# Optimization experiments

Measured on AMD Instinct MI355X. Metric: run time of the kernel, lower is better.

Reference implementation:

```python
import jax, jax.numpy as jnp
import numpy as np
from jax import lax

B, T, D, H, V, L = 32, 64, 512, 512, 32000, 2
EOS, PAD = 3, 0
SAMPLE_SEED = 42


def setup_inputs() -> dict:
    key = jax.random.key(0)
    ks = jax.random.split(key, 10)
    s = 0.05
    return {
        "input_seq": jax.random.normal(ks[0], (B, T, D), dtype=jnp.float32),
        "h_encode": jax.random.normal(ks[1], (L, B, H), dtype=jnp.float32),
        "c_encode": jax.random.normal(ks[2], (L, B, H), dtype=jnp.float32),
        # stacked per-layer LSTM cell params (layer0 in=D, layer>=1 in=H; D==H so stackable)
        "W_ih": jax.random.normal(ks[3], (L, 4 * H, D), dtype=jnp.float32) * s,
        "W_hh": jax.random.normal(ks[4], (L, 4 * H, H), dtype=jnp.float32) * s,
        "b_ih": jnp.zeros((L, 4 * H), dtype=jnp.float32),
        "b_hh": jnp.zeros((L, 4 * H), dtype=jnp.float32),
        "fc_w": jax.random.normal(ks[5], (V, H), dtype=jnp.float32) * s,
        "fc_b": jnp.zeros((V,), dtype=jnp.float32),
        "embed": jax.random.normal(ks[6], (V, D), dtype=jnp.float32) * s,
    }


def _lstm_cell(x, h, c, wi, wh, bi, bh):
    # gates in torch LSTMCell order: i, f, g, o
    g = x @ wi.T + bi + h @ wh.T + bh  # [B, 4H]
    i, f, gg, o = jnp.split(g, 4, axis=-1)
    i, f, o = jax.nn.sigmoid(i), jax.nn.sigmoid(f), jax.nn.sigmoid(o)
    c2 = f * c + i * jnp.tanh(gg)
    h2 = o * jnp.tanh(c2)
    return h2, c2


def reference(input_seq, h_encode, c_encode, W_ih, W_hh, b_ih, b_hh, fc_w, fc_b, embed):
    n_layers = h_encode.shape[0]
    seq = jnp.swapaxes(input_seq, 0, 1)  # [T, B, D]
    batch = input_seq.shape[0]

    def step(carry, t):
        h, c, finished, x = carry
        inp = x
        hs, cs = [], []
        for l in range(n_layers):  # fixed small layer loop
            hl, cl = _lstm_cell(inp, h[l], c[l], W_ih[l], W_hh[l], b_ih[l], b_hh[l])
            hs.append(hl)
            cs.append(cl)
            inp = hl
        h2 = jnp.stack(hs)
        c2 = jnp.stack(cs)
        logits = inp @ fc_w.T + fc_b  # [B, V]; temperature=1.0 is identity
        key = jax.random.fold_in(jax.random.key(SAMPLE_SEED), t)
        sampled = jax.random.categorical(key, logits, axis=-1)  # multinomial(softmax(logits))
        token = jnp.where(finished, PAD, sampled)
        finished2 = finished | (sampled == EOS)
        next_x = embed[token]  # [B, D] feedback embedding (no teacher forcing)
        return (h2, c2, finished2, next_x), (logits, token)

    carry0 = (h_encode, c_encode, jnp.zeros((batch,), dtype=bool), seq[0])
    _, (logits_t, tokens_t) = lax.scan(step, carry0, jnp.arange(seq.shape[0]))
    outputs = jnp.swapaxes(logits_t, 0, 1)  # [B, T, V]
    tokens = jnp.swapaxes(tokens_t, 0, 1)  # [B, T]
    return outputs, tokens
```

## Files before the change

kernel.cpp:

```cpp
#include <hip/hip_runtime.h>
#include <cstdint>
#include <cstddef>

#define B_  32
#define T_  64
#define D_  512
#define H_  512
#define V_  32000
#define NPART 8

__device__ float g_x[B_ * D_];
__device__ float g_h[2][2 * B_ * H_];
__device__ float g_c[2][2 * B_ * H_];
__device__ float g_pval[B_ * NPART];
__device__ int   g_pidx[B_ * NPART];
__device__ int   g_fin[B_];
__device__ float g_wT[512 * 32000];
__device__ float g_wLT[2][1024 * 2048];
__device__ float g_part[64][B_][2048];
__device__ float g_lpart[8][B_][V_];

__host__ __device__ __forceinline__ void threefry2x32(uint32_t k0, uint32_t k1,
                                                      uint32_t x0, uint32_t x1,
                                                      uint32_t& o0, uint32_t& o1) {
  uint32_t kx = k0 ^ k1 ^ 0x1BD11BDAu;
  x0 += k0; x1 += k1;
#define RND(r) { x0 += x1; x1 = (x1 << (r)) | (x1 >> (32 - (r))); x1 ^= x0; }
  RND(13) RND(15) RND(26) RND(6)  x0 += k1; x1 += kx + 1u;
  RND(17) RND(29) RND(16) RND(24) x0 += kx; x1 += k0 + 2u;
  RND(13) RND(15) RND(26) RND(6)  x0 += k0; x1 += k1 + 3u;
  RND(17) RND(29) RND(16) RND(24) x0 += k1; x1 += kx + 4u;
  RND(13) RND(15) RND(26) RND(6)  x0 += kx; x1 += k0 + 5u;
#undef RND
  o0 = x0; o1 = x1;
}

__device__ __forceinline__ float gumbel_from_u32(uint32_t bits) {
  float f = __uint_as_float((bits >> 9) | 0x3f800000u) - 1.0f;
  const float TINY = 1.1754943508222875e-38f;
  float u = f * (1.0f - TINY) + TINY;
  u = fmaxf(u, TINY);
  return -logf(-logf(u));
}

__device__ __forceinline__ void fma4(float4& a, const float4 w, float s) {
  a.x += w.x * s; a.y += w.y * s; a.z += w.z * s; a.w += w.w * s;
}

__global__ void init_kernel(const float* __restrict__ input_seq,
                            const float* __restrict__ h_enc,
                            const float* __restrict__ c_enc) {
  int i = blockIdx.x * 256 + threadIdx.x;
  if (i < B_ * D_) g_x[i] = input_seq[(size_t)(i >> 9) * (T_ * D_) + (i & 511)];
  if (i < 2 * B_ * H_) { g_h[0][i] = h_enc[i]; g_c[0][i] = c_enc[i]; }
  if (i < B_) g_fin[i] = 0;
}

__global__ void transpose_kernel(const float* __restrict__ src, int R, int which) {
  float* dst;
  switch (which) {
    case 0:  dst = g_wT; break;
    case 1:  dst = g_wLT[0]; break;
    case 2:  dst = g_wLT[0] + 512 * 2048; break;
    case 3:  dst = g_wLT[1]; break;
    default: dst = g_wLT[1] + 512 * 2048; break;
  }
  __shared__ float tile[64][65];
  const int r0 = blockIdx.x * 64;
  const int c0 = blockIdx.y * 64;
  const int tx = threadIdx.x & 63;
  const int ty = threadIdx.x >> 6;
#pragma unroll
  for (int i = 0; i < 16; ++i) {
    const int row = ty + 4 * i;
    tile[row][tx] = src[(size_t)(r0 + row) * 512 + c0 + tx];
  }
  __syncthreads();
#pragma unroll
  for (int i = 0; i < 16; ++i) {
    const int row = ty + 4 * i;
    dst[(size_t)(c0 + row) * R + r0 + tx] = tile[tx][row];
  }
}

__global__ void lstm_part_kernel(int cur, int layer) {
  const int blk = blockIdx.x;
  const int kslo = blk & 7, bg = (blk >> 3) & 3, kshi = blk >> 5;
  const int ks = kslo + 8 * kshi;
  const int tid = threadIdx.x;
  const int b0 = bg * 8;

  const float* z = (ks < 32) ? ((layer == 0) ? g_x : &g_h[cur ^ 1][0])
                             : &g_h[cur][layer * B_ * H_];
  const int k0 = (ks & 31) * 16;

  __shared__ float zs[8][16];
  if (tid < 128) zs[tid >> 4][tid & 15] = z[(b0 + (tid >> 4)) * 512 + k0 + (tid & 15)];
  __syncthreads();

  float4 accA[8], accB[8];
#pragma unroll
  for (int b = 0; b < 8; ++b) { accA[b] = make_float4(0,0,0,0); accB[b] = make_float4(0,0,0,0); }

  for (int kk = 0; kk < 16; ++kk) {
    const float4* w4 = (const float4*)&g_wLT[layer][(size_t)(ks * 16 + kk) * 2048];
    float4 wa = w4[tid], wb = w4[tid + 256];
#pragma unroll
    for (int b = 0; b < 8; ++b) {
      float zb = zs[b][kk];
      fma4(accA[b], wa, zb);
      fma4(accB[b], wb, zb);
    }
  }
#pragma unroll
  for (int b = 0; b < 8; ++b) {
    float4* p = (float4*)&g_part[ks][b0 + b][0];
    p[tid]       = accA[b];
    p[tid + 256] = accB[b];
  }
}

__global__ void lstm_finish_kernel(int cur, int layer,
                                   const float* __restrict__ bih,
                                   const float* __restrict__ bhh) {
  const int gid = blockIdx.x * 256 + threadIdx.x;
  const int b = gid >> 9, j = gid & 511;
  float gi = 0.f, gf = 0.f, gg = 0.f, go = 0.f;
#pragma unroll 8
  for (int ks = 0; ks < 64; ++ks) {
    gi += g_part[ks][b][j];
    gf += g_part[ks][b][512 + j];
    gg += g_part[ks][b][1024 + j];
    go += g_part[ks][b][1536 + j];
  }
  gi += bih[j]          + bhh[j];
  gf += bih[512 + j]    + bhh[512 + j];
  gg += bih[1024 + j]   + bhh[1024 + j];
  go += bih[1536 + j]   + bhh[1536 + j];

  const float* c_in = &g_c[cur][layer * B_ * H_];
  float* h_out = &g_h[cur ^ 1][layer * B_ * H_];
  float* c_out = &g_c[cur ^ 1][layer * B_ * H_];
  float c0 = c_in[b * H_ + j];
  float si = 1.f / (1.f + expf(-gi));
  float sf = 1.f / (1.f + expf(-gf));
  float so = 1.f / (1.f + expf(-go));
  float cn = sf * c0 + si * tanhf(gg);
  float hn = so * tanhf(cn);
  c_out[b * H_ + j] = cn;
  h_out[b * H_ + j] = hn;
}

__global__ void logits_part_kernel(int cur) {
  const int blk = blockIdx.x;
  const int vt = blk % 63, ks = blk / 63;
  const int tid = threadIdx.x;
  const int k0 = ks * 64;

  __shared__ float hs[32 * 64];
  const float* h2 = &g_h[cur ^ 1][B_ * H_];
  {
    float4* d4 = (float4*)hs;
#pragma unroll
    for (int i = 0; i < 2; ++i) {
      const int f4i = tid + i * 256;
      d4[f4i] = ((const float4*)h2)[(f4i >> 4) * 128 + (k0 >> 2) + (f4i & 15)];
    }
  }
  __syncthreads();

  const int v0 = vt * 512 + tid * 2;
  if (v0 >= V_) return;

  float2 acc[32];
#pragma unroll
  for (int b = 0; b < 32; ++b) acc[b] = make_float2(0.f, 0.f);

  for (int k = 0; k < 64; ++k) {
    float2 w = *(const float2*)&g_wT[(size_t)(k0 + k) * V_ + v0];
#pragma unroll
    for (int b = 0; b < 32; ++b) {
      float hb = hs[b * 64 + k];
      acc[b].x += w.x * hb;
      acc[b].y += w.y * hb;
    }
  }
#pragma unroll
  for (int b = 0; b < 32; ++b)
    *(float2*)&g_lpart[ks][b][v0] = acc[b];
}

__global__ void logits_combine_kernel(const float* __restrict__ fc_b,
                                      float* __restrict__ out_logits,
                                      int t, uint32_t key0, uint32_t key1) {
  __shared__ float sv[256];
  __shared__ int   si[256];
  const int b  = blockIdx.x >> 3;
  const int vr = blockIdx.x & 7;
  const int tid = threadIdx.x;
  const int vend = (vr + 1) * 4000;

  float best = -3.0e38f; int bidx = 0x7fffffff;
  for (int it = 0; it < 16; ++it) {
    const int v = vr * 4000 + it * 256 + tid;
    if (v < vend) {
      float s = 0.f;
#pragma unroll
      for (int ks = 0; ks < 8; ++ks) s += g_lpart[ks][b][v];
      float lv = s + fc_b[v];
      out_logits[(size_t)(b * T_ + t) * V_ + v] = lv;
      uint32_t y0, y1;
      threefry2x32(key0, key1, 0u, (uint32_t)(b * V_ + v), y0, y1);
      float val = lv + gumbel_from_u32(y0 ^ y1);
      if (val > best) { best = val; bidx = v; }
    }
  }
  sv[tid] = best; si[tid] = bidx;
  __syncthreads();
  for (int s = 128; s > 0; s >>= 1) {
    if (tid < s) {
      float ov = sv[tid + s]; int oi = si[tid + s];
      if (ov > sv[tid] || (ov == sv[tid] && oi < si[tid])) { sv[tid] = ov; si[tid] = oi; }
    }
    __syncthreads();
  }
  if (tid == 0) { g_pval[b * NPART + vr] = sv[0]; g_pidx[b * NPART + vr] = si[0]; }
}

__global__ void sample_kernel(const float* __restrict__ embed,
                              float* __restrict__ out_tokens, int t) {
  __shared__ int stok;
  const int b = blockIdx.x;
  const int tid = threadIdx.x;
  if (tid == 0) {
    float best = -3.0e38f; int bidx = 0x7fffffff;
    for (int p = 0; p < NPART; ++p) {
      float v = g_pval[b * NPART + p];
      int  ix = g_pidx[b * NPART + p];
      if (v > best || (v == best && ix < bidx)) { best = v; bidx = ix; }
    }
    int sampled = bidx;
    if (sampled < 0) sampled = 0;
    if (sampled >= V_) sampled = V_ - 1;
    int fin = g_fin[b];
    int token = fin ? 0 : sampled;
    out_tokens[b * T_ + t] = (float)token;
    g_fin[b] = fin | (sampled == 3 ? 1 : 0);
    stok = token;
  }
  __syncthreads();
  const int token = stok;
  const float4* er = (const float4*)(embed + (size_t)token * D_);
  float4* xr = (float4*)(g_x + b * D_);
  if (tid < 128) xr[tid] = er[tid];
}

extern "C" void kernel_launch(void* const* d_in, const int* in_sizes, int n_in,
                              void* d_out, int out_size, void* d_ws, size_t ws_size,
                              hipStream_t stream) {
  const float* input_seq = (const float*)d_in[0];
  const float* h_enc = (const float*)d_in[1];
  const float* c_enc = (const float*)d_in[2];
  const float* Wih   = (const float*)d_in[3];
  const float* Whh   = (const float*)d_in[4];
  const float* bih   = (const float*)d_in[5];
  const float* bhh   = (const float*)d_in[6];
  const float* fc_w  = (const float*)d_in[7];
  const float* fc_b  = (const float*)d_in[8];
  const float* embed = (const float*)d_in[9];
  float* out = (float*)d_out;
  float* tok_out = out + (size_t)B_ * T_ * V_;
  (void)d_ws; (void)ws_size;

  init_kernel<<<128, 256, 0, stream>>>(input_seq, h_enc, c_enc);

  transpose_kernel<<<dim3(500, 8), 256, 0, stream>>>(fc_w, 32000, 0);
  transpose_kernel<<<dim3(32, 8),  256, 0, stream>>>(Wih,                      2048, 1);
  transpose_kernel<<<dim3(32, 8),  256, 0, stream>>>(Whh,                      2048, 2);
  transpose_kernel<<<dim3(32, 8),  256, 0, stream>>>(Wih + (size_t)2048 * 512, 2048, 3);
  transpose_kernel<<<dim3(32, 8),  256, 0, stream>>>(Whh + (size_t)2048 * 512, 2048, 4);

  uint32_t keys[T_][2];
  for (int t = 0; t < T_; ++t)
    threefry2x32(0u, 42u, 0u, (uint32_t)t, keys[t][0], keys[t][1]);

  int cur = 0;
  for (int t = 0; t < T_; ++t) {
    lstm_part_kernel<<<256, 256, 0, stream>>>(cur, 0);
    lstm_finish_kernel<<<64, 256, 0, stream>>>(cur, 0, bih, bhh);
    lstm_part_kernel<<<256, 256, 0, stream>>>(cur, 1);
    lstm_finish_kernel<<<64, 256, 0, stream>>>(cur, 1, bih + 2048, bhh + 2048);
    logits_part_kernel<<<504, 256, 0, stream>>>(cur);
    logits_combine_kernel<<<256, 256, 0, stream>>>(fc_b, out, t, keys[t][0], keys[t][1]);
    sample_kernel<<<B_, 256, 0, stream>>>(embed, tok_out, t);
    cur ^= 1;
  }
}
```

Before: 6.051 ms.

## Fuse sampling into LSTM input staging and hoist layer-1 recurrent matmul early

```diff
diff --git a/kernel.cpp b/kernel.cpp
--- a/kernel.cpp
+++ b/kernel.cpp
@@ -7,18 +7,17 @@
 #define D_  512
 #define H_  512
 #define V_  32000
-#define NPART 8
-
-__device__ float g_x[B_ * D_];
+#define GATES 2048
+
 __device__ float g_h[2][2 * B_ * H_];
 __device__ float g_c[2][2 * B_ * H_];
-__device__ float g_pval[B_ * NPART];
-__device__ int   g_pidx[B_ * NPART];
-__device__ int   g_fin[B_];
+__device__ int   g_fin[2][B_];
+__device__ unsigned long long g_best[B_];
 __device__ float g_wT[512 * 32000];
 __device__ float g_wLT[2][1024 * 2048];
-__device__ float g_part[64][B_][2048];
-__device__ float g_lpart[8][B_][V_];
+__device__ float g_part0[16][B_][GATES];
+__device__ float g_part1[24][B_][GATES];
+__device__ float g_lpart[4][B_][V_];
 
 __host__ __device__ __forceinline__ void threefry2x32(uint32_t k0, uint32_t k1,
                                                       uint32_t x0, uint32_t x1,
@@ -43,17 +42,11 @@
   return -logf(-logf(u));
 }
 
-__device__ __forceinline__ void fma4(float4& a, const float4 w, float s) {
-  a.x += w.x * s; a.y += w.y * s; a.z += w.z * s; a.w += w.w * s;
-}
-
-__global__ void init_kernel(const float* __restrict__ input_seq,
-                            const float* __restrict__ h_enc,
+__global__ void init_kernel(const float* __restrict__ h_enc,
                             const float* __restrict__ c_enc) {
   int i = blockIdx.x * 256 + threadIdx.x;
-  if (i < B_ * D_) g_x[i] = input_seq[(size_t)(i >> 9) * (T_ * D_) + (i & 511)];
   if (i < 2 * B_ * H_) { g_h[0][i] = h_enc[i]; g_c[0][i] = c_enc[i]; }
-  if (i < B_) g_fin[i] = 0;
+  if (i < B_) { g_fin[0][i] = 0; g_fin[1][i] = 0; }
 }
 
 __global__ void transpose_kernel(const float* __restrict__ src, int R, int which) {
@@ -83,60 +76,135 @@
   }
 }
 
-__global__ void lstm_part_kernel(int cur, int layer) {
+template<int PER>
+__device__ __forceinline__ void stage_t(float* __restrict__ zs,
+                                        const float* __restrict__ row,
+                                        int kq, int b) {
+#pragma unroll
+  for (int i = 0; i < PER; i += 4) {
+    const float4 v = *(const float4*)&row[kq * PER + i];
+    const int kk = kq * PER + i;
+    zs[(kk + 0) * 32 + b] = v.x;
+    zs[(kk + 1) * 32 + b] = v.y;
+    zs[(kk + 2) * 32 + b] = v.z;
+    zs[(kk + 3) * 32 + b] = v.w;
+  }
+}
+
+template<int KS>
+__device__ __forceinline__ void mm_part(const float* __restrict__ wrow,
+                                        float* __restrict__ pout,
+                                        const float* __restrict__ zs,
+                                        int j0, int tid) {
+  float2 acc[32];
+#pragma unroll
+  for (int b = 0; b < 32; ++b) acc[b] = make_float2(0.f, 0.f);
+#pragma unroll 4
+  for (int k = 0; k < KS; ++k) {
+    const float2 w = *(const float2*)&wrow[(size_t)k * GATES + j0 + 2 * tid];
+    const float4* z4 = (const float4*)&zs[k * 32];
+#pragma unroll
+    for (int bq = 0; bq < 8; ++bq) {
+      const float4 z = z4[bq];
+      acc[bq * 4 + 0].x += w.x * z.x; acc[bq * 4 + 0].y += w.y * z.x;
+      acc[bq * 4 + 1].x += w.x * z.y; acc[bq * 4 + 1].y += w.y * z.y;
+      acc[bq * 4 + 2].x += w.x * z.z; acc[bq * 4 + 2].y += w.y * z.z;
+      acc[bq * 4 + 3].x += w.x * z.w; acc[bq * 4 + 3].y += w.y * z.w;
+    }
+  }
+#pragma unroll
+  for (int b = 0; b < 32; ++b)
+    *(float2*)&pout[(size_t)b * GATES + j0 + 2 * tid] = acc[b];
+}
+
+__device__ __forceinline__ int unpack_v(unsigned long long bb) {
+  int v = (int)(0xFFFFFFFFu - (uint32_t)(bb & 0xFFFFFFFFu));
+  if (v < 0) v = 0;
+  if (v >= V_) v = V_ - 1;
+  return v;
+}
+
+__global__ void parts_a_kernel(int cur, int t,
+                               const float* __restrict__ input_seq,
+                               const float* __restrict__ embed,
+                               float* __restrict__ out_tokens) {
+  __shared__ __align__(16) float zs[64 * 32];
+  __shared__ int stok[B_];
+  const int tid = threadIdx.x;
   const int blk = blockIdx.x;
-  const int kslo = blk & 7, bg = (blk >> 3) & 3, kshi = blk >> 5;
-  const int ks = kslo + 8 * kshi;
-  const int tid = threadIdx.x;
-  const int b0 = bg * 8;
-
-  const float* z = (ks < 32) ? ((layer == 0) ? g_x : &g_h[cur ^ 1][0])
-                             : &g_h[cur][layer * B_ * H_];
-  const int k0 = (ks & 31) * 16;
-
-  __shared__ float zs[8][16];
-  if (tid < 128) zs[tid >> 4][tid & 15] = z[(b0 + (tid >> 4)) * 512 + k0 + (tid & 15)];
+  const int b = tid >> 3, kq = tid & 7;
+
+  if (blk < 64) {
+    const int ks = blk >> 2, jt = blk & 3;
+    const int k0 = ks * 64, j0 = jt * 512;
+    if (k0 < 512) {
+      if (t == 0) {
+        const float* row = &input_seq[(size_t)b * (T_ * D_)];
+        stage_t<8>(zs, row + k0, kq, b);
+      } else {
+        if (tid < B_) {
+          unsigned long long bb = g_best[tid];
+          int v = unpack_v(bb);
+          int fin = g_fin[(t + 1) & 1][tid];
+          int tok = fin ? 0 : v;
+          stok[tid] = tok;
+          if (blk == 0) {
+            out_tokens[(size_t)tid * T_ + (t - 1)] = (float)tok;
+            g_fin[t & 1][tid] = fin | (v == 3 ? 1 : 0);
+          }
+        }
+        __syncthreads();
+        const float* row = &embed[(size_t)stok[b] * D_];
+        stage_t<8>(zs, row + k0, kq, b);
+      }
+    } else {
+      const float* row = &g_h[cur][0 * B_ * H_ + b * H_];
+      stage_t<8>(zs, row + (k0 - 512), kq, b);
+    }
+    __syncthreads();
+    mm_part<64>(&g_wLT[0][(size_t)k0 * GATES], &g_part0[ks][0][0], zs, j0, tid);
+  } else {
+    const int bb2 = blk - 64;
+    const int ks = bb2 >> 2, jt = bb2 & 3;
+    const int k0 = ks * 64, j0 = jt * 512;
+    const float* row = &g_h[cur][1 * B_ * H_ + b * H_];
+    stage_t<8>(zs, row + k0, kq, b);
+    __syncthreads();
+    mm_part<64>(&g_wLT[1][(size_t)(512 + k0) * GATES], &g_part1[16 + ks][0][0],
+                zs, j0, tid);
+  }
+}
+
+__global__ void parts_l1x_kernel(int cur) {
+  __shared__ __align__(16) float zs[32 * 32];
+  const int tid = threadIdx.x;
+  const int ks = blockIdx.x >> 2, jt = blockIdx.x & 3;
+  const int k0 = ks * 32, j0 = jt * 512;
+  const int b = tid >> 3, kq = tid & 7;
+  const float* row = &g_h[cur ^ 1][0 * B_ * H_ + b * H_];
+  stage_t<4>(zs, row + k0, kq, b);
   __syncthreads();
-
-  float4 accA[8], accB[8];
-#pragma unroll
-  for (int b = 0; b < 8; ++b) { accA[b] = make_float4(0,0,0,0); accB[b] = make_float4(0,0,0,0); }
-
-  for (int kk = 0; kk < 16; ++kk) {
-    const float4* w4 = (const float4*)&g_wLT[layer][(size_t)(ks * 16 + kk) * 2048];
-    float4 wa = w4[tid], wb = w4[tid + 256];
-#pragma unroll
-    for (int b = 0; b < 8; ++b) {
-      float zb = zs[b][kk];
-      fma4(accA[b], wa, zb);
-      fma4(accB[b], wb, zb);
-    }
-  }
-#pragma unroll
-  for (int b = 0; b < 8; ++b) {
-    float4* p = (float4*)&g_part[ks][b0 + b][0];
-    p[tid]       = accA[b];
-    p[tid + 256] = accB[b];
-  }
-}
-
-__global__ void lstm_finish_kernel(int cur, int layer,
+  mm_part<32>(&g_wLT[1][(size_t)k0 * GATES], &g_part1[ks][0][0], zs, j0, tid);
+}
+
+__global__ void lstm_finish_kernel(int cur, int layer, int nslots,
                                    const float* __restrict__ bih,
                                    const float* __restrict__ bhh) {
   const int gid = blockIdx.x * 256 + threadIdx.x;
   const int b = gid >> 9, j = gid & 511;
+  const float* P = (layer == 0) ? &g_part0[0][0][0] : &g_part1[0][0][0];
   float gi = 0.f, gf = 0.f, gg = 0.f, go = 0.f;
-#pragma unroll 8
-  for (int ks = 0; ks < 64; ++ks) {
-    gi += g_part[ks][b][j];
-    gf += g_part[ks][b][512 + j];
-    gg += g_part[ks][b][1024 + j];
-    go += g_part[ks][b][1536 + j];
-  }
-  gi += bih[j]          + bhh[j];
-  gf += bih[512 + j]    + bhh[512 + j];
-  gg += bih[1024 + j]   + bhh[1024 + j];
-  go += bih[1536 + j]   + bhh[1536 + j];
+  for (int s = 0; s < nslots; ++s) {
+    const float* p = P + (size_t)s * B_ * GATES + (size_t)b * GATES;
+    gi += p[j];
+    gf += p[512 + j];
+    gg += p[1024 + j];
+    go += p[1536 + j];
+  }
+  gi += bih[j]        + bhh[j];
+  gf += bih[512 + j]  + bhh[512 + j];
+  gg += bih[1024 + j] + bhh[1024 + j];
+  go += bih[1536 + j] + bhh[1536 + j];
 
   const float* c_in = &g_c[cur][layer * B_ * H_];
   float* h_out = &g_h[cur ^ 1][layer * B_ * H_];
@@ -152,20 +220,18 @@
 }
 
 __global__ void logits_part_kernel(int cur) {
+  __shared__ __align__(16) float hs[128 * 32];
   const int blk = blockIdx.x;
   const int vt = blk % 63, ks = blk / 63;
   const int tid = threadIdx.x;
-  const int k0 = ks * 64;
-
-  __shared__ float hs[32 * 64];
-  const float* h2 = &g_h[cur ^ 1][B_ * H_];
+  const int k0 = ks * 128;
+
+  if (blk == 0 && tid < B_) g_best[tid] = 0ull;
+
   {
-    float4* d4 = (float4*)hs;
-#pragma unroll
-    for (int i = 0; i < 2; ++i) {
-      const int f4i = tid + i * 256;
-      d4[f4i] = ((const float4*)h2)[(f4i >> 4) * 128 + (k0 >> 2) + (f4i & 15)];
-    }
+    const int b = tid >> 3, kq = tid & 7;
+    const float* row = &g_h[cur ^ 1][B_ * H_ + b * H_];
+    stage_t<16>(hs, row + k0, kq, b);
   }
   __syncthreads();
 
@@ -175,14 +241,17 @@
   float2 acc[32];
 #pragma unroll
   for (int b = 0; b < 32; ++b) acc[b] = make_float2(0.f, 0.f);
-
-  for (int k = 0; k < 64; ++k) {
-    float2 w = *(const float2*)&g_wT[(size_t)(k0 + k) * V_ + v0];
-#pragma unroll
-    for (int b = 0; b < 32; ++b) {
-      float hb = hs[b * 64 + k];
-      acc[b].x += w.x * hb;
-      acc[b].y += w.y * hb;
+#pragma unroll 4
+  for (int k = 0; k < 128; ++k) {
+    const float2 w = *(const float2*)&g_wT[(size_t)(k0 + k) * V_ + v0];
+    const float4* z4 = (const float4*)&hs[k * 32];
+#pragma unroll
+    for (int bq = 0; bq < 8; ++bq) {
+      const float4 z = z4[bq];
+      acc[bq * 4 + 0].x += w.x * z.x; acc[bq * 4 + 0].y += w.y * z.x;
+      acc[bq * 4 + 1].x += w.x * z.y; acc[bq * 4 + 1].y += w.y * z.y;
+      acc[bq * 4 + 2].x += w.x * z.z; acc[bq * 4 + 2].y += w.y * z.z;
+      acc[bq * 4 + 3].x += w.x * z.w; acc[bq * 4 + 3].y += w.y * z.w;
     }
   }
 #pragma unroll
@@ -193,66 +262,47 @@
 __global__ void logits_combine_kernel(const float* __restrict__ fc_b,
                                       float* __restrict__ out_logits,
                                       int t, uint32_t key0, uint32_t key1) {
-  __shared__ float sv[256];
-  __shared__ int   si[256];
+  __shared__ unsigned long long sv[256];
   const int b  = blockIdx.x >> 3;
   const int vr = blockIdx.x & 7;
   const int tid = threadIdx.x;
   const int vend = (vr + 1) * 4000;
 
-  float best = -3.0e38f; int bidx = 0x7fffffff;
+  unsigned long long best = 0ull;
   for (int it = 0; it < 16; ++it) {
     const int v = vr * 4000 + it * 256 + tid;
     if (v < vend) {
-      float s = 0.f;
-#pragma unroll
-      for (int ks = 0; ks < 8; ++ks) s += g_lpart[ks][b][v];
+      float s = g_lpart[0][b][v] + g_lpart[1][b][v]
+              + g_lpart[2][b][v] + g_lpart[3][b][v];
       float lv = s + fc_b[v];
       out_logits[(size_t)(b * T_ + t) * V_ + v] = lv;
       uint32_t y0, y1;
       threefry2x32(key0, key1, 0u, (uint32_t)(b * V_ + v), y0, y1);
       float val = lv + gumbel_from_u32(y0 ^ y1);
-      if (val > best) { best = val; bidx = v; }
+      uint32_t u = __float_as_uint(val);
+      u ^= (u >> 31) ? 0xFFFFFFFFu : 0x80000000u;
+      unsigned long long pk =
+          ((unsigned long long)u << 32) | (unsigned long long)(0xFFFFFFFFu - (uint32_t)v);
+      if (pk > best) best = pk;
     }
   }
-  sv[tid] = best; si[tid] = bidx;
+  sv[tid] = best;
   __syncthreads();
   for (int s = 128; s > 0; s >>= 1) {
-    if (tid < s) {
-      float ov = sv[tid + s]; int oi = si[tid + s];
-      if (ov > sv[tid] || (ov == sv[tid] && oi < si[tid])) { sv[tid] = ov; si[tid] = oi; }
-    }
+    if (tid < s) { if (sv[tid + s] > sv[tid]) sv[tid] = sv[tid + s]; }
     __syncthreads();
   }
-  if (tid == 0) { g_pval[b * NPART + vr] = sv[0]; g_pidx[b * NPART + vr] = si[0]; }
-}
-
-__global__ void sample_kernel(const float* __restrict__ embed,
-                              float* __restrict__ out_tokens, int t) {
-  __shared__ int stok;
-  const int b = blockIdx.x;
-  const int tid = threadIdx.x;
-  if (tid == 0) {
-    float best = -3.0e38f; int bidx = 0x7fffffff;
-    for (int p = 0; p < NPART; ++p) {
-      float v = g_pval[b * NPART + p];
-      int  ix = g_pidx[b * NPART + p];
-      if (v > best || (v == best && ix < bidx)) { best = v; bidx = ix; }
-    }
-    int sampled = bidx;
-    if (sampled < 0) sampled = 0;
-    if (sampled >= V_) sampled = V_ - 1;
-    int fin = g_fin[b];
-    int token = fin ? 0 : sampled;
-    out_tokens[b * T_ + t] = (float)token;
-    g_fin[b] = fin | (sampled == 3 ? 1 : 0);
-    stok = token;
-  }
-  __syncthreads();
-  const int token = stok;
-  const float4* er = (const float4*)(embed + (size_t)token * D_);
-  float4* xr = (float4*)(g_x + b * D_);
-  if (tid < 128) xr[tid] = er[tid];
+  if (tid == 0) atomicMax(&g_best[b], sv[0]);
+}
+
+__global__ void finalize_kernel(float* __restrict__ out_tokens) {
+  const int tid = threadIdx.x;
+  if (tid < B_) {
+    int v = unpack_v(g_best[tid]);
+    int fin = g_fin[(T_ + 1) & 1][tid];
+    int tok = fin ? 0 : v;
+    out_tokens[(size_t)tid * T_ + (T_ - 1)] = (float)tok;
+  }
 }
 
 extern "C" void kernel_launch(void* const* d_in, const int* in_sizes, int n_in,
@@ -270,9 +320,9 @@
   const float* embed = (const float*)d_in[9];
   float* out = (float*)d_out;
   float* tok_out = out + (size_t)B_ * T_ * V_;
-  (void)d_ws; (void)ws_size;
-
-  init_kernel<<<128, 256, 0, stream>>>(input_seq, h_enc, c_enc);
+  (void)d_ws; (void)ws_size; (void)in_sizes; (void)n_in; (void)out_size;
+
+  init_kernel<<<128, 256, 0, stream>>>(h_enc, c_enc);
 
   transpose_kernel<<<dim3(500, 8), 256, 0, stream>>>(fc_w, 32000, 0);
   transpose_kernel<<<dim3(32, 8),  256, 0, stream>>>(Wih,                      2048, 1);
@@ -286,13 +336,13 @@
 
   int cur = 0;
   for (int t = 0; t < T_; ++t) {
-    lstm_part_kernel<<<256, 256, 0, stream>>>(cur, 0);
-    lstm_finish_kernel<<<64, 256, 0, stream>>>(cur, 0, bih, bhh);
-    lstm_part_kernel<<<256, 256, 0, stream>>>(cur, 1);
-    lstm_finish_kernel<<<64, 256, 0, stream>>>(cur, 1, bih + 2048, bhh + 2048);
-    logits_part_kernel<<<504, 256, 0, stream>>>(cur);
+    parts_a_kernel<<<96, 256, 0, stream>>>(cur, t, input_seq, embed, tok_out);
+    lstm_finish_kernel<<<64, 256, 0, stream>>>(cur, 0, 16, bih, bhh);
+    parts_l1x_kernel<<<64, 256, 0, stream>>>(cur);
+    lstm_finish_kernel<<<64, 256, 0, stream>>>(cur, 1, 24, bih + 2048, bhh + 2048);
+    logits_part_kernel<<<252, 256, 0, stream>>>(cur);
     logits_combine_kernel<<<256, 256, 0, stream>>>(fc_b, out, t, keys[t][0], keys[t][1]);
-    sample_kernel<<<B_, 256, 0, stream>>>(embed, tok_out, t);
     cur ^= 1;
   }
-}
+  finalize_kernel<<<1, 64, 0, stream>>>(tok_out);
+}
```

Result: slower. 6.330 ms (+4.6%).

## Fuse LSTM split-K, logits, and sampling into fewer kernels with atomic argmax

Applied to the files above, without the earlier changes.

```diff
diff --git a/kernel.cpp b/kernel.cpp
--- a/kernel.cpp
+++ b/kernel.cpp
@@ -7,18 +7,14 @@
 #define D_  512
 #define H_  512
 #define V_  32000
-#define NPART 8
-
-__device__ float g_x[B_ * D_];
+#define GATES 2048
+
 __device__ float g_h[2][2 * B_ * H_];
 __device__ float g_c[2][2 * B_ * H_];
-__device__ float g_pval[B_ * NPART];
-__device__ int   g_pidx[B_ * NPART];
-__device__ int   g_fin[B_];
+__device__ int   g_fin[2][B_];
+__device__ unsigned long long g_best2[2][B_][8];
 __device__ float g_wT[512 * 32000];
 __device__ float g_wLT[2][1024 * 2048];
-__device__ float g_part[64][B_][2048];
-__device__ float g_lpart[8][B_][V_];
 
 __host__ __device__ __forceinline__ void threefry2x32(uint32_t k0, uint32_t k1,
                                                       uint32_t x0, uint32_t x1,
@@ -43,17 +39,24 @@
   return -logf(-logf(u));
 }
 
-__device__ __forceinline__ void fma4(float4& a, const float4 w, float s) {
-  a.x += w.x * s; a.y += w.y * s; a.z += w.z * s; a.w += w.w * s;
-}
-
-__global__ void init_kernel(const float* __restrict__ input_seq,
-                            const float* __restrict__ h_enc,
+__device__ __forceinline__ int unpack_v(unsigned long long bb) {
+  int v = (int)(0xFFFFFFFFu - (uint32_t)(bb & 0xFFFFFFFFu));
+  if (v < 0) v = 0;
+  if (v >= V_) v = V_ - 1;
+  return v;
+}
+
+__device__ __forceinline__ unsigned long long ullmax(unsigned long long a,
+                                                     unsigned long long b) {
+  return a > b ? a : b;
+}
+
+__global__ void init_kernel(const float* __restrict__ h_enc,
                             const float* __restrict__ c_enc) {
   int i = blockIdx.x * 256 + threadIdx.x;
-  if (i < B_ * D_) g_x[i] = input_seq[(size_t)(i >> 9) * (T_ * D_) + (i & 511)];
   if (i < 2 * B_ * H_) { g_h[0][i] = h_enc[i]; g_c[0][i] = c_enc[i]; }
-  if (i < B_) g_fin[i] = 0;
+  if (i < B_) { g_fin[0][i] = 0; g_fin[1][i] = 0; }
+  if (i < 2 * B_ * 8) ((unsigned long long*)g_best2)[i] = 0ull;
 }
 
 __global__ void transpose_kernel(const float* __restrict__ src, int R, int which) {
@@ -83,176 +86,188 @@
   }
 }
 
-__global__ void lstm_part_kernel(int cur, int layer) {
-  const int blk = blockIdx.x;
-  const int kslo = blk & 7, bg = (blk >> 3) & 3, kshi = blk >> 5;
-  const int ks = kslo + 8 * kshi;
+__global__ __launch_bounds__(512) void lstm_cell_kernel(
+    int layer, int cur, int tt,
+    const float* __restrict__ input_seq, const float* __restrict__ embed,
+    const float* __restrict__ bih, const float* __restrict__ bhh,
+    float* __restrict__ out_tokens) {
+  __shared__ __align__(16) float zs[16 * 512];
+  __shared__ float gl[4][16][16];
+  __shared__ int stok[16];
   const int tid = threadIdx.x;
-  const int b0 = bg * 8;
-
-  const float* z = (ks < 32) ? ((layer == 0) ? g_x : &g_h[cur ^ 1][0])
-                             : &g_h[cur][layer * B_ * H_];
-  const int k0 = (ks & 31) * 16;
-
-  __shared__ float zs[8][16];
-  if (tid < 128) zs[tid >> 4][tid & 15] = z[(b0 + (tid >> 4)) * 512 + k0 + (tid & 15)];
+  const int jt = blockIdx.x & 31, bh = blockIdx.x >> 5;
+  const int j0 = jt * 16, b0 = bh * 16;
+
+  if (layer == 0 && tt > 0) {
+    const int ps = (tt - 1) & 1;
+    if (tid < 16) {
+      const int b = b0 + tid;
+      unsigned long long m = 0ull;
+#pragma unroll
+      for (int s = 0; s < 8; ++s) m = ullmax(m, g_best2[ps][b][s]);
+      const int v = unpack_v(m);
+      const int fin = g_fin[ps ^ 1][b];
+      const int tok = fin ? 0 : v;
+      stok[tid] = tok;
+      if (jt == 0) {
+        out_tokens[(size_t)b * T_ + (tt - 1)] = (float)tok;
+        g_fin[ps][b] = fin | (v == 3 ? 1 : 0);
+      }
+    }
+    if (jt == 0 && tid < 128)
+      g_best2[tt & 1][b0 + (tid >> 3)][tid & 7] = 0ull;
+    __syncthreads();
+  }
+
+  const int jp = tid & 7, gg_ = (tid >> 3) & 3, lb = tid >> 5;
+  const float* wbase = &g_wLT[layer][(size_t)gg_ * 512 + j0 + jp * 2];
+  float2 acc = make_float2(0.f, 0.f);
+
+  for (int p = 0; p < 2; ++p) {
+    {
+      const int slb = tid & 15, kq = tid >> 4;
+      const float* src;
+      if (layer == 0) {
+        src = (p == 0)
+          ? ((tt == 0) ? &input_seq[(size_t)(b0 + slb) * T_ * D_]
+                       : &embed[(size_t)stok[slb] * D_])
+          : &g_h[cur][0 * B_ * H_ + (b0 + slb) * H_];
+      } else {
+        src = (p == 0) ? &g_h[cur ^ 1][0 * B_ * H_ + (b0 + slb) * H_]
+                       : &g_h[cur][1 * B_ * H_ + (b0 + slb) * H_];
+      }
+#pragma unroll
+      for (int i = 0; i < 16; i += 4) {
+        const float4 v = *(const float4*)&src[kq * 16 + i];
+        *(float4*)&zs[slb * 512 + kq * 16 + i] = v;
+      }
+    }
+    __syncthreads();
+    const float* wrow = wbase + (size_t)p * 512 * GATES;
+    const float* zrow = &zs[lb * 512];
+#pragma unroll 8
+    for (int k = 0; k < 512; ++k) {
+      const float2 w = *(const float2*)&wrow[(size_t)k * GATES];
+      const float z = zrow[k];
+      acc.x += w.x * z; acc.y += w.y * z;
+    }
+    __syncthreads();
+  }
+
+  *(float2*)&gl[gg_][lb][jp * 2] = acc;
   __syncthreads();
-
-  float4 accA[8], accB[8];
-#pragma unroll
-  for (int b = 0; b < 8; ++b) { accA[b] = make_float4(0,0,0,0); accB[b] = make_float4(0,0,0,0); }
-
-  for (int kk = 0; kk < 16; ++kk) {
-    const float4* w4 = (const float4*)&g_wLT[layer][(size_t)(ks * 16 + kk) * 2048];
-    float4 wa = w4[tid], wb = w4[tid + 256];
-#pragma unroll
-    for (int b = 0; b < 8; ++b) {
-      float zb = zs[b][kk];
-      fma4(accA[b], wa, zb);
-      fma4(accB[b], wb, zb);
-    }
-  }
-#pragma unroll
-  for (int b = 0; b < 8; ++b) {
-    float4* p = (float4*)&g_part[ks][b0 + b][0];
-    p[tid]       = accA[b];
-    p[tid + 256] = accB[b];
-  }
-}
-
-__global__ void lstm_finish_kernel(int cur, int layer,
-                                   const float* __restrict__ bih,
-                                   const float* __restrict__ bhh) {
-  const int gid = blockIdx.x * 256 + threadIdx.x;
-  const int b = gid >> 9, j = gid & 511;
-  float gi = 0.f, gf = 0.f, gg = 0.f, go = 0.f;
-#pragma unroll 8
-  for (int ks = 0; ks < 64; ++ks) {
-    gi += g_part[ks][b][j];
-    gf += g_part[ks][b][512 + j];
-    gg += g_part[ks][b][1024 + j];
-    go += g_part[ks][b][1536 + j];
-  }
-  gi += bih[j]          + bhh[j];
-  gf += bih[512 + j]    + bhh[512 + j];
-  gg += bih[1024 + j]   + bhh[1024 + j];
-  go += bih[1536 + j]   + bhh[1536 + j];
-
-  const float* c_in = &g_c[cur][layer * B_ * H_];
-  float* h_out = &g_h[cur ^ 1][layer * B_ * H_];
-  float* c_out = &g_c[cur ^ 1][layer * B_ * H_];
-  float c0 = c_in[b * H_ + j];
-  float si = 1.f / (1.f + expf(-gi));
-  float sf = 1.f / (1.f + expf(-gf));
-  float so = 1.f / (1.f + expf(-go));
-  float cn = sf * c0 + si * tanhf(gg);
-  float hn = so * tanhf(cn);
-  c_out[b * H_ + j] = cn;
-  h_out[b * H_ + j] = hn;
-}
-
-__global__ void logits_part_kernel(int cur) {
-  const int blk = blockIdx.x;
-  const int vt = blk % 63, ks = blk / 63;
+  if (tid < 256) {
+    const int lb2 = tid >> 4, jj = tid & 15;
+    const int j = j0 + jj, b = b0 + lb2;
+    float gi = gl[0][lb2][jj] + bih[j]        + bhh[j];
+    float gf = gl[1][lb2][jj] + bih[512 + j]  + bhh[512 + j];
+    float gg = gl[2][lb2][jj] + bih[1024 + j] + bhh[1024 + j];
+    float go = gl[3][lb2][jj] + bih[1536 + j] + bhh[1536 + j];
+    const float c0v = g_c[cur][layer * B_ * H_ + b * H_ + j];
+    const float si = 1.f / (1.f + expf(-gi));
+    const float sf = 1.f / (1.f + expf(-gf));
+    const float so = 1.f / (1.f + expf(-go));
+    const float cn = sf * c0v + si * tanhf(gg);
+    const float hn = so * tanhf(cn);
+    g_c[cur ^ 1][layer * B_ * H_ + b * H_ + j] = cn;
+    g_h[cur ^ 1][layer * B_ * H_ + b * H_ + j] = hn;
+  }
+}
+
+__global__ __launch_bounds__(512) void logits_kernel(
+    int cur, int tt, const float* __restrict__ fc_b,
+    float* __restrict__ out_logits, uint32_t key0, uint32_t key1) {
+  __shared__ __align__(16) float hs[256 * 32];
   const int tid = threadIdx.x;
-  const int k0 = ks * 64;
-
-  __shared__ float hs[32 * 64];
-  const float* h2 = &g_h[cur ^ 1][B_ * H_];
-  {
-    float4* d4 = (float4*)hs;
-#pragma unroll
-    for (int i = 0; i < 2; ++i) {
-      const int f4i = tid + i * 256;
-      d4[f4i] = ((const float4*)h2)[(f4i >> 4) * 128 + (k0 >> 2) + (f4i & 15)];
-    }
-  }
-  __syncthreads();
-
-  const int v0 = vt * 512 + tid * 2;
-  if (v0 >= V_) return;
-
-  float2 acc[32];
-#pragma unroll
-  for (int b = 0; b < 32; ++b) acc[b] = make_float2(0.f, 0.f);
-
-  for (int k = 0; k < 64; ++k) {
-    float2 w = *(const float2*)&g_wT[(size_t)(k0 + k) * V_ + v0];
-#pragma unroll
-    for (int b = 0; b < 32; ++b) {
-      float hb = hs[b * 64 + k];
-      acc[b].x += w.x * hb;
-      acc[b].y += w.y * hb;
-    }
-  }
-#pragma unroll
-  for (int b = 0; b < 32; ++b)
-    *(float2*)&g_lpart[ks][b][v0] = acc[b];
-}
-
-__global__ void logits_combine_kernel(const float* __restrict__ fc_b,
-                                      float* __restrict__ out_logits,
-                                      int t, uint32_t key0, uint32_t key1) {
-  __shared__ float sv[256];
-  __shared__ int   si[256];
-  const int b  = blockIdx.x >> 3;
-  const int vr = blockIdx.x & 7;
+  const int v0 = blockIdx.x * 128;
+  const int vp = tid & 63, bg = tid >> 6;
+  const int v = v0 + vp * 2;
+
+  float2 a0 = {0.f,0.f}, a1 = {0.f,0.f}, a2 = {0.f,0.f}, a3 = {0.f,0.f};
+
+  for (int p = 0; p < 2; ++p) {
+    {
+      const int b = tid & 31, kq = tid >> 5;
+      const float* src = &g_h[cur ^ 1][B_ * H_ + b * H_ + p * 256 + kq * 16];
+#pragma unroll
+      for (int i = 0; i < 16; i += 4) {
+        const float4 w = *(const float4*)&src[i];
+        const int k = kq * 16 + i;
+        hs[(k + 0) * 32 + b] = w.x;
+        hs[(k + 1) * 32 + b] = w.y;
+        hs[(k + 2) * 32 + b] = w.z;
+        hs[(k + 3) * 32 + b] = w.w;
+      }
+    }
+    __syncthreads();
+    const float* wrow = &g_wT[(size_t)(p * 256) * V_ + v];
+#pragma unroll 4
+    for (int k = 0; k < 256; ++k) {
+      const float2 w = *(const float2*)&wrow[(size_t)k * V_];
+      const float4 z = *(const float4*)&hs[k * 32 + bg * 4];
+      a0.x += w.x * z.x; a0.y += w.y * z.x;
+      a1.x += w.x * z.y; a1.y += w.y * z.y;
+      a2.x += w.x * z.z; a2.y += w.y * z.z;
+      a3.x += w.x * z.w; a3.y += w.y * z.w;
+    }
+    __syncthreads();
+  }
+
+  const float bi0 = fc_b[v], bi1 = fc_b[v + 1];
+  const int bb0 = bg * 4;
+  unsigned long long m0, m1, m2, m3;
+#define DOPACK(ACC, BIDX, MOUT) {                                              \
+    const float l0 = ACC.x + bi0, l1 = ACC.y + bi1;                            \
+    *(float2*)&out_logits[(size_t)((BIDX) * T_ + tt) * V_ + v] =               \
+        make_float2(l0, l1);                                                   \
+    uint32_t y0, y1;                                                           \
+    threefry2x32(key0, key1, 0u, (uint32_t)((BIDX) * V_ + v), y0, y1);         \
+    const float val0 = l0 + gumbel_from_u32(y0 ^ y1);                          \
+    threefry2x32(key0, key1, 0u, (uint32_t)((BIDX) * V_ + v + 1), y0, y1);     \
+    const float val1 = l1 + gumbel_from_u32(y0 ^ y1);                          \
+    uint32_t u0 = __float_as_uint(val0);                                       \
+    u0 ^= (u0 >> 31) ? 0xFFFFFFFFu : 0x80000000u;                              \
+    uint32_t u1 = __float_as_uint(val1);                                       \
+    u1 ^= (u1 >> 31) ? 0xFFFFFFFFu : 0x80000000u;                              \
+    const unsigned long long p0 =                                              \
+        ((unsigned long long)u0 << 32) | (unsigned long long)(0xFFFFFFFFu - (uint32_t)v);       \
+    const unsigned long long p1 =                                              \
+        ((unsigned long long)u1 << 32) | (unsigned long long)(0xFFFFFFFFu - (uint32_t)(v + 1)); \
+    MOUT = p0 > p1 ? p0 : p1;                                                  \
+  }
+  DOPACK(a0, bb0 + 0, m0)
+  DOPACK(a1, bb0 + 1, m1)
+  DOPACK(a2, bb0 + 2, m2)
+  DOPACK(a3, bb0 + 3, m3)
+#undef DOPACK
+
+#pragma unroll
+  for (int off = 1; off < 64; off <<= 1) {
+    m0 = ullmax(m0, (unsigned long long)__shfl_xor(m0, off));
+    m1 = ullmax(m1, (unsigned long long)__shfl_xor(m1, off));
+    m2 = ullmax(m2, (unsigned long long)__shfl_xor(m2, off));
+    m3 = ullmax(m3, (unsigned long long)__shfl_xor(m3, off));
+  }
+  if ((tid & 63) == 0) {
+    const int slot = blockIdx.x & 7;
+    atomicMax(&g_best2[tt & 1][bb0 + 0][slot], m0);
+    atomicMax(&g_best2[tt & 1][bb0 + 1][slot], m1);
+    atomicMax(&g_best2[tt & 1][bb0 + 2][slot], m2);
+    atomicMax(&g_best2[tt & 1][bb0 + 3][slot], m3);
+  }
+}
+
+__global__ void finalize_kernel(float* __restrict__ out_tokens) {
   const int tid = threadIdx.x;
-  const int vend = (vr + 1) * 4000;
-
-  float best = -3.0e38f; int bidx = 0x7fffffff;
-  for (int it = 0; it < 16; ++it) {
-    const int v = vr * 4000 + it * 256 + tid;
-    if (v < vend) {
-      float s = 0.f;
-#pragma unroll
-      for (int ks = 0; ks < 8; ++ks) s += g_lpart[ks][b][v];
-      float lv = s + fc_b[v];
-      out_logits[(size_t)(b * T_ + t) * V_ + v] = lv;
-      uint32_t y0, y1;
-      threefry2x32(key0, key1, 0u, (uint32_t)(b * V_ + v), y0, y1);
-      float val = lv + gumbel_from_u32(y0 ^ y1);
-      if (val > best) { best = val; bidx = v; }
-    }
-  }
-  sv[tid] = best; si[tid] = bidx;
-  __syncthreads();
-  for (int s = 128; s > 0; s >>= 1) {
-    if (tid < s) {
-      float ov = sv[tid + s]; int oi = si[tid + s];
-      if (ov > sv[tid] || (ov == sv[tid] && oi < si[tid])) { sv[tid] = ov; si[tid] = oi; }
-    }
-    __syncthreads();
-  }
-  if (tid == 0) { g_pval[b * NPART + vr] = sv[0]; g_pidx[b * NPART + vr] = si[0]; }
-}
-
-__global__ void sample_kernel(const float* __restrict__ embed,
-                              float* __restrict__ out_tokens, int t) {
-  __shared__ int stok;
-  const int b = blockIdx.x;
-  const int tid = threadIdx.x;
-  if (tid == 0) {
-    float best = -3.0e38f; int bidx = 0x7fffffff;
-    for (int p = 0; p < NPART; ++p) {
-      float v = g_pval[b * NPART + p];
-      int  ix = g_pidx[b * NPART + p];
-      if (v > best || (v == best && ix < bidx)) { best = v; bidx = ix; }
-    }
-    int sampled = bidx;
-    if (sampled < 0) sampled = 0;
-    if (sampled >= V_) sampled = V_ - 1;
-    int fin = g_fin[b];
-    int token = fin ? 0 : sampled;
-    out_tokens[b * T_ + t] = (float)token;
-    g_fin[b] = fin | (sampled == 3 ? 1 : 0);
-    stok = token;
-  }
-  __syncthreads();
-  const int token = stok;
-  const float4* er = (const float4*)(embed + (size_t)token * D_);
-  float4* xr = (float4*)(g_x + b * D_);
-  if (tid < 128) xr[tid] = er[tid];
+  if (tid < B_) {
+    const int ps = (T_ - 1) & 1;
+    unsigned long long m = 0ull;
+#pragma unroll
+    for (int s = 0; s < 8; ++s) m = ullmax(m, g_best2[ps][tid][s]);
+    const int v = unpack_v(m);
+    const int fin = g_fin[ps ^ 1][tid];
+    out_tokens[(size_t)tid * T_ + (T_ - 1)] = (float)(fin ? 0 : v);
+  }
 }
 
 extern "C" void kernel_launch(void* const* d_in, const int* in_sizes, int n_in,
@@ -270,9 +285,9 @@
   const float* embed = (const float*)d_in[9];
   float* out = (float*)d_out;
   float* tok_out = out + (size_t)B_ * T_ * V_;
-  (void)d_ws; (void)ws_size;
-
-  init_kernel<<<128, 256, 0, stream>>>(input_seq, h_enc, c_enc);
+  (void)d_ws; (void)ws_size; (void)in_sizes; (void)n_in; (void)out_size;
+
+  init_kernel<<<128, 256, 0, stream>>>(h_enc, c_enc);
 
   transpose_kernel<<<dim3(500, 8), 256, 0, stream>>>(fc_w, 32000, 0);
   transpose_kernel<<<dim3(32, 8),  256, 0, stream>>>(Wih,                      2048, 1);
@@ -286,13 +301,13 @@
 
   int cur = 0;
   for (int t = 0; t < T_; ++t) {
-    lstm_part_kernel<<<256, 256, 0, stream>>>(cur, 0);
-    lstm_finish_kernel<<<64, 256, 0, stream>>>(cur, 0, bih, bhh);
-    lstm_part_kernel<<<256, 256, 0, stream>>>(cur, 1);
-    lstm_finish_kernel<<<64, 256, 0, stream>>>(cur, 1, bih + 2048, bhh + 2048);
-    logits_part_kernel<<<504, 256, 0, stream>>>(cur);
-    logits_combine_kernel<<<256, 256, 0, stream>>>(fc_b, out, t, keys[t][0], keys[t][1]);
-    sample_kernel<<<B_, 256, 0, stream>>>(embed, tok_out, t);
+    lstm_cell_kernel<<<64, 512, 0, stream>>>(0, cur, t, input_seq, embed,
+                                             bih, bhh, tok_out);
+    lstm_cell_kernel<<<64, 512, 0, stream>>>(1, cur, t, input_seq, embed,
+                                             bih + 2048, bhh + 2048, tok_out);
+    logits_kernel<<<250, 512, 0, stream>>>(cur, t, fc_b, out,
+                                           keys[t][0], keys[t][1]);
     cur ^= 1;
   }
-}
+  finalize_kernel<<<1, 64, 0, stream>>>(tok_out);
+}
```

Result: slower. 11.45 ms (+89.3%).
